# Kernel optimization log

Hardware: AMD Instinct MI355X
Metric: run time of the kernel (lower is better)

Reference implementation:

```python
import jax, jax.numpy as jnp
import numpy as np

B, L, E = 4, 2048, 1024
H, D = 16, 64  # heads, head_dim; H*D == E


def setup_inputs() -> dict:
    key = jax.random.key(0)
    ks = jax.random.split(key, 6)
    s = 0.02
    return {
        "x": jax.random.normal(ks[0], (B, L, E), dtype=jnp.float32),
        "Wq": jax.random.normal(ks[1], (E, H * D), dtype=jnp.float32) * s,
        "Wk": jax.random.normal(ks[2], (E, H * D), dtype=jnp.float32) * s,
        "Wv": jax.random.normal(ks[3], (E, H * D), dtype=jnp.float32) * s,
        "Wo": jax.random.normal(ks[4], (H * D, E), dtype=jnp.float32) * s,
        "bo": jax.random.normal(ks[5], (E,), dtype=jnp.float32) * s,
    }


def reference(x, Wq, Wk, Wv, Wo, bo):
    b, l, e = x.shape
    q = (x @ Wq).reshape(b, l, H, D)
    k = (x @ Wk).reshape(b, l, H, D)
    v = (x @ Wv).reshape(b, l, H, D)
    # NOTE: original scales by sqrt(embed_size), not sqrt(head_dim)
    energy = jnp.einsum('nqhd,nkhd->nhqk', q, k)
    attn = jax.nn.softmax(energy / jnp.sqrt(jnp.float32(e)), axis=3)
    out = jnp.einsum('nhql,nlhd->nqhd', attn, v).reshape(b, l, H * D)
    return out @ Wo + bo
```

## Files before the change

kernel.cpp:

```cpp
#include <hip/hip_runtime.h>

#define B_ 4
#define L_ 2048
#define E_ 1024
#define H_ 16
#define D_ 64
#define CSCALE 0.045084960222629414f

typedef short s16x8 __attribute__((ext_vector_type(8)));
typedef short s16x4 __attribute__((ext_vector_type(4)));
typedef float f32x4 __attribute__((ext_vector_type(4)));

__device__ __forceinline__ unsigned short f2bf(float f) {
  union { float f; unsigned int u; } v;
  v.f = f;
  unsigned int u = v.u;
  u += 0x7fffu + ((u >> 16) & 1u);
  return (unsigned short)(u >> 16);
}

__device__ __forceinline__ void async16(const void* g, void* l) {
  __builtin_amdgcn_global_load_lds(
      (__attribute__((address_space(1))) void*)(g),
      (__attribute__((address_space(3))) void*)(l), 16, 0, 0);
}

__global__ void k_prep(const float* __restrict__ x,
                       const float* __restrict__ Wq, const float* __restrict__ Wk,
                       const float* __restrict__ Wv, const float* __restrict__ Wo,
                       unsigned short* __restrict__ xb,
                       unsigned short* __restrict__ Wt, unsigned short* __restrict__ WoT) {
  __shared__ float t[32][33];
  int bid = blockIdx.x, tid = threadIdx.x;
  if (bid < 8192) {
    int i = bid * 256 + tid;
    float4 v = ((const float4*)x)[i];
    ushort4 o;
    o.x = f2bf(v.x); o.y = f2bf(v.y); o.z = f2bf(v.z); o.w = f2bf(v.w);
    ((ushort4*)xb)[i] = o;
    return;
  }
  int tt = bid - 8192;
  int wsel = tt >> 10, tile = tt & 1023;
  const float* in = (wsel == 0) ? Wq : (wsel == 1) ? Wk : (wsel == 2) ? Wv : Wo;
  unsigned short* out = (wsel == 0) ? Wt : (wsel == 1) ? Wt + (1u << 20)
                        : (wsel == 2) ? Wt + (2u << 20) : WoT;
  int bx = tile & 31, by = tile >> 5;
  int tx = tid & 31, ty = tid >> 5;
  int xcol = bx * 32 + tx;
  int y0 = by * 32;
#pragma unroll
  for (int i = 0; i < 4; ++i)
    t[ty + i * 8][tx] = in[(size_t)(y0 + ty + i * 8) * 1024 + xcol];
  __syncthreads();
  int xo = by * 32 + tx;
  int yo0 = bx * 32;
#pragma unroll
  for (int i = 0; i < 4; ++i)
    out[(size_t)(yo0 + ty + i * 8) * 1024 + xo] = f2bf(t[tx][ty + i * 8]);
}

__global__ __launch_bounds__(512) void k_gemm_qkvt(
    const unsigned short* __restrict__ xb, const unsigned short* __restrict__ Wt,
    unsigned short* __restrict__ Qb, unsigned short* __restrict__ Kb,
    unsigned short* __restrict__ Vt) {
  __shared__ __align__(16) unsigned short St[3][12288];
  const int bid0 = blockIdx.x;
  const int bid = (bid0 & 7) * 96 + (bid0 >> 3);
  const int tid = threadIdx.x;
  const int w = tid >> 6, lane = tid & 63;
  const int quad = lane >> 4, mrow = lane & 15;
  const bool isQK = bid < 512;
  int m0, n0;
  const unsigned short *PA, *PB;
  if (isQK) {
    m0 = (bid & 31) * 256;
    n0 = (bid >> 5) * 128;
    PA = xb + (size_t)m0 * 1024;
    PB = Wt + (size_t)n0 * 1024;
  } else {
    int g = bid - 512;
    m0 = (g & 3) * 256;
    n0 = (g >> 2) * 128;
    PA = Wt + (2u << 20) + (size_t)m0 * 1024;
    PB = xb + (size_t)n0 * 1024;
  }
  const int wr = (w >> 1) * 64, wc = (w & 1) * 64;

  auto issue = [&](int kt, int s) {
    int ktw = kt & 31;
#pragma unroll
    for (int r = 0; r < 2; ++r) {
      int c = r * 512 + tid;
      int row = c >> 2, cl = c & 3, gc = cl ^ (row & 3);
      async16(PA + (size_t)row * 1024 + ktw * 32 + gc * 8, &St[s][c * 8]);
    }
    {
      int c = tid;
      int row = c >> 2, cl = c & 3, gc = cl ^ (row & 3);
      async16(PB + (size_t)row * 1024 + ktw * 32 + gc * 8, &St[s][8192 + c * 8]);
    }
  };

  const f32x4 fz = {0.f, 0.f, 0.f, 0.f};
  f32x4 acc[4][4];
#pragma unroll
  for (int a = 0; a < 4; ++a)
#pragma unroll
    for (int b = 0; b < 4; ++b) acc[a][b] = fz;

  issue(0, 0);
  issue(1, 1);

  for (int kt = 0; kt < 32; ++kt) {
    asm volatile("s_waitcnt vmcnt(3)" ::: "memory");
    __builtin_amdgcn_s_barrier();
    asm volatile("" ::: "memory");
    issue(kt + 2, (kt + 2) % 3);
    const unsigned short* As = &St[kt % 3][0];
    const unsigned short* Bs = &St[kt % 3][8192];
    s16x8 a[4], b[4];
#pragma unroll
    for (int mt = 0; mt < 4; ++mt) {
      int row = wr + mt * 16 + mrow;
      a[mt] = *(const s16x8*)&As[row * 32 + ((quad ^ (row & 3)) << 3)];
    }
#pragma unroll
    for (int nt = 0; nt < 4; ++nt) {
      int row = wc + nt * 16 + mrow;
      b[nt] = *(const s16x8*)&Bs[row * 32 + ((quad ^ (row & 3)) << 3)];
    }
#pragma unroll
    for (int mt = 0; mt < 4; ++mt)
#pragma unroll
      for (int nt = 0; nt < 4; ++nt)
        acc[mt][nt] = __builtin_amdgcn_mfma_f32_16x16x32_bf16(a[mt], b[nt], acc[mt][nt], 0, 0, 0);
  }
  if (isQK) {
#pragma unroll
    for (int mt = 0; mt < 4; ++mt)
#pragma unroll
      for (int nt = 0; nt < 4; ++nt)
#pragma unroll
        for (int i = 0; i < 4; ++i) {
          int row = m0 + wr + mt * 16 + quad * 4 + i;
          int col = n0 + wc + nt * 16 + mrow;
          int bb = row >> 11, l = row & 2047;
          if (col < 1024) {
            int h = col >> 6, d = col & 63;
            Qb[(((size_t)(bb * 16 + h)) * 2048 + l) * 64 + d] = f2bf(acc[mt][nt][i]);
          } else {
            int c2 = col - 1024, h = c2 >> 6, d = c2 & 63;
            Kb[(((size_t)(bb * 16 + h)) * 2048 + l) * 64 + d] = f2bf(acc[mt][nt][i] * CSCALE);
          }
        }
  } else {
#pragma unroll
    for (int mt = 0; mt < 4; ++mt)
#pragma unroll
      for (int nt = 0; nt < 4; ++nt)
#pragma unroll
        for (int i = 0; i < 4; ++i) {
          int f = m0 + wr + mt * 16 + quad * 4 + i;
          int tk = n0 + wc + nt * 16 + mrow;
          int bb = tk >> 11, l = tk & 2047;
          Vt[((size_t)(bb * 1024 + f)) * 2048 + l] = f2bf(acc[mt][nt][i]);
        }
  }
}

struct AK { s16x8 k0, k1; };
struct ST { f32x4 s0, s1; };
struct PAT { s16x4 n0, n1; };

__device__ __forceinline__ AK load_ak(const unsigned short* Kt, int mt, int mrow, int quad) {
  int row = mt * 16 + mrow;
  AK r;
  r.k0 = *(const s16x8*)&Kt[row * 64 + (((0 + quad) ^ (row & 7)) << 3)];
  r.k1 = *(const s16x8*)&Kt[row * 64 + (((4 + quad) ^ (row & 7)) << 3)];
  return r;
}

__device__ __forceinline__ ST qkmm(const AK& a, const s16x8 (&qb)[2][2]) {
  const f32x4 fz = {0.f, 0.f, 0.f, 0.f};
  ST t; t.s0 = fz; t.s1 = fz;
  __builtin_amdgcn_s_setprio(1);
  t.s0 = __builtin_amdgcn_mfma_f32_16x16x32_bf16(a.k0, qb[0][0], t.s0, 0, 0, 0);
  t.s1 = __builtin_amdgcn_mfma_f32_16x16x32_bf16(a.k0, qb[1][0], t.s1, 0, 0, 0);
  t.s0 = __builtin_amdgcn_mfma_f32_16x16x32_bf16(a.k1, qb[0][1], t.s0, 0, 0, 0);
  t.s1 = __builtin_amdgcn_mfma_f32_16x16x32_bf16(a.k1, qb[1][1], t.s1, 0, 0, 0);
  __builtin_amdgcn_s_setprio(0);
  return t;
}

__device__ __forceinline__ s16x4 exp_pack(const f32x4 sv, float& lracc) {
  float p0 = __builtin_amdgcn_exp2f(sv[0]);
  float p1 = __builtin_amdgcn_exp2f(sv[1]);
  float p2 = __builtin_amdgcn_exp2f(sv[2]);
  float p3 = __builtin_amdgcn_exp2f(sv[3]);
  lracc += (p0 + p1) + (p2 + p3);
  unsigned int r01, r23;
  asm("v_cvt_pk_bf16_f32 %0, %1, %2" : "=v"(r01) : "v"(p0), "v"(p1));
  asm("v_cvt_pk_bf16_f32 %0, %1, %2" : "=v"(r23) : "v"(p2), "v"(p3));
  union { unsigned int u[2]; s16x4 v4; } uu;
  uu.u[0] = r01; uu.u[1] = r23;
  return uu.v4;
}

__device__ __forceinline__ PAT expp(const ST& t, float (&lr)[2]) {
  PAT r;
  r.n0 = exp_pack(t.s0, lr[0]);
  r.n1 = exp_pack(t.s1, lr[1]);
  return r;
}

__device__ __forceinline__ void pv(const unsigned short* Vs, int lt, const PAT& p,
                                   f32x4 (&o)[2][4], int mrow, int quad) {
  s16x4 vb[4];
  int lbase = lt * 16 + quad * 4;
  int cg = lbase >> 3, off = lbase & 7;
#pragma unroll
  for (int dt = 0; dt < 4; ++dt) {
    int row = dt * 16 + mrow;
    vb[dt] = *(const s16x4*)&Vs[row * 64 + ((cg ^ (row & 7)) << 3) + off];
  }
  __builtin_amdgcn_s_setprio(1);
#pragma unroll
  for (int dt = 0; dt < 4; ++dt) {
    o[0][dt] = __builtin_amdgcn_mfma_f32_16x16x16bf16_1k(p.n0, vb[dt], o[0][dt], 0, 0, 0);
    o[1][dt] = __builtin_amdgcn_mfma_f32_16x16x16bf16_1k(p.n1, vb[dt], o[1][dt], 0, 0, 0);
  }
  __builtin_amdgcn_s_setprio(0);
}

__global__ __launch_bounds__(512) void k_attn(
    const unsigned short* __restrict__ Qb, const unsigned short* __restrict__ Kb,
    const unsigned short* __restrict__ Vt, unsigned short* __restrict__ AO) {
  __shared__ __align__(16) unsigned short KVs[3][8192];
  const int tid = threadIdx.x, w = tid >> 6, lane = tid & 63;
  const int quad = lane >> 4, mrow = lane & 15;
  const int lin = blockIdx.x + 8 * blockIdx.y;
  const int swz = (lin & 7) * 64 + (lin >> 3);
  const int bh = swz >> 3;
  const int q0 = (swz & 7) * 256;
  const unsigned short* Qh = Qb + (size_t)bh * 2048 * 64;
  const unsigned short* Kh = Kb + (size_t)bh * 2048 * 64;
  const unsigned short* Vh = Vt + (size_t)bh * 64 * 2048;
  unsigned short* KVf = &KVs[0][0];

#pragma unroll
  for (int r = 0; r < 4; ++r) {
    int c = r * 512 + tid;
    int row = c >> 3, cl = c & 7;
    int gc = cl ^ (row & 7);
    async16(Qh + (size_t)(q0 + row) * 64 + gc * 8, &KVf[c * 8]);
  }
  asm volatile("s_waitcnt vmcnt(0)" ::: "memory");
  __builtin_amdgcn_s_barrier();
  asm volatile("" ::: "memory");
  s16x8 qb[2][2];
#pragma unroll
  for (int nt = 0; nt < 2; ++nt)
#pragma unroll
    for (int ks = 0; ks < 2; ++ks) {
      int row = w * 32 + nt * 16 + mrow;
      qb[nt][ks] = *(const s16x8*)&KVf[row * 64 + (((ks * 4 + quad) ^ (row & 7)) << 3)];
    }
  asm volatile("" ::: "memory");
  __builtin_amdgcn_s_barrier();
  asm volatile("" ::: "memory");

  {
    int row = tid >> 3, cl = tid & 7, gc = cl ^ (row & 7);
    async16(Kh + (size_t)row * 64 + gc * 8, &KVs[0][tid * 8]);
    async16(Vh + (size_t)row * 2048 + gc * 8, &KVs[0][4096 + tid * 8]);
    async16(Kh + (size_t)(64 + row) * 64 + gc * 8, &KVs[1][tid * 8]);
    async16(Vh + (size_t)row * 2048 + 64 + gc * 8, &KVs[1][4096 + tid * 8]);
  }

  const f32x4 fz = {0.f, 0.f, 0.f, 0.f};
  f32x4 o[2][4];
  float lr[2];
#pragma unroll
  for (int nt = 0; nt < 2; ++nt) {
    lr[nt] = 0.f;
#pragma unroll
    for (int dt = 0; dt < 4; ++dt) o[nt][dt] = fz;
  }

  for (int j = 0; j < 32; ++j) {
    asm volatile("s_waitcnt vmcnt(2)" ::: "memory");
    __builtin_amdgcn_s_barrier();
    asm volatile("" ::: "memory");
    {
      int jj = (j + 2) & 31;
      unsigned short* nb = &KVs[(j + 2) % 3][0];
      int row = tid >> 3, cl = tid & 7, gc = cl ^ (row & 7);
      async16(Kh + (size_t)(jj * 64 + row) * 64 + gc * 8, &nb[tid * 8]);
      async16(Vh + (size_t)row * 2048 + jj * 64 + gc * 8, &nb[4096 + tid * 8]);
    }
    const unsigned short* Kt = &KVs[j % 3][0];
    const unsigned short* Vs = &KVs[j % 3][4096];

    AK a0 = load_ak(Kt, 0, mrow, quad); ST t0 = qkmm(a0, qb);
    AK a1 = load_ak(Kt, 1, mrow, quad); ST t1 = qkmm(a1, qb);
    PAT p0 = expp(t0, lr);
    AK a2 = load_ak(Kt, 2, mrow, quad); ST t2 = qkmm(a2, qb);
    pv(Vs, 0, p0, o, mrow, quad);
    PAT p1 = expp(t1, lr);
    AK a3 = load_ak(Kt, 3, mrow, quad); ST t3 = qkmm(a3, qb);
    pv(Vs, 1, p1, o, mrow, quad);
    PAT p2 = expp(t2, lr);
    pv(Vs, 2, p2, o, mrow, quad);
    PAT p3 = expp(t3, lr);
    pv(Vs, 3, p3, o, mrow, quad);
  }

#pragma unroll
  for (int nt = 0; nt < 2; ++nt) {
    float v = lr[nt];
    v += __shfl_xor(v, 16);
    v += __shfl_xor(v, 32);
    lr[nt] = v;
  }

  int b_ = bh >> 4, h = bh & 15;
#pragma unroll
  for (int nt = 0; nt < 2; ++nt)
#pragma unroll
    for (int i = 0; i < 4; ++i) {
      float inv = 1.f / __shfl(lr[nt], quad * 4 + i, 64);
      int qrow = q0 + w * 32 + nt * 16 + quad * 4 + i;
#pragma unroll
      for (int dt = 0; dt < 4; ++dt) {
        int d = dt * 16 + mrow;
        AO[((size_t)(b_ * 2048 + qrow)) * 1024 + h * 64 + d] = f2bf(o[nt][dt][i] * inv);
      }
    }
}

__global__ __launch_bounds__(512) void k_gemm_out(
    const unsigned short* __restrict__ Ab, const unsigned short* __restrict__ WoT,
    const float* __restrict__ bo, float* __restrict__ out) {
  __shared__ __align__(16) unsigned short St[3][8192];
  const int tid = threadIdx.x;
  const int w = tid >> 6, lane = tid & 63;
  const int quad = lane >> 4, mrow = lane & 15;
  const int lin = blockIdx.x + 64 * blockIdx.y;
  const int swz = (lin & 7) * 64 + (lin >> 3);
  const int m0 = (swz & 63) * 128, n0 = (swz >> 6) * 128;
  const int wr = (w >> 1) * 32, wc = (w & 1) * 64;
  const unsigned short* PA = Ab + (size_t)m0 * 1024;
  const unsigned short* PB = WoT + (size_t)n0 * 1024;

  auto issue = [&](int kt, int s) {
    int ktw = kt & 31;
    {
      int c = tid;
      int row = c >> 2, cl = c & 3, gc = cl ^ (row & 3);
      async16(PA + (size_t)row * 1024 + ktw * 32 + gc * 8, &St[s][c * 8]);
    }
    {
      int c = tid;
      int row = c >> 2, cl = c & 3, gc = cl ^ (row & 3);
      async16(PB + (size_t)row * 1024 + ktw * 32 + gc * 8, &St[s][4096 + c * 8]);
    }
  };

  const f32x4 fz = {0.f, 0.f, 0.f, 0.f};
  f32x4 acc[2][4];
#pragma unroll
  for (int a = 0; a < 2; ++a)
#pragma unroll
    for (int b = 0; b < 4; ++b) acc[a][b] = fz;

  issue(0, 0);
  issue(1, 1);

  for (int kt = 0; kt < 32; ++kt) {
    asm volatile("s_waitcnt vmcnt(2)" ::: "memory");
    __builtin_amdgcn_s_barrier();
    asm volatile("" ::: "memory");
    issue(kt + 2, (kt + 2) % 3);
    const unsigned short* As = &St[kt % 3][0];
    const unsigned short* Bs = &St[kt % 3][4096];
    s16x8 a[2], b[4];
#pragma unroll
    for (int mt = 0; mt < 2; ++mt) {
      int row = wr + mt * 16 + mrow;
      a[mt] = *(const s16x8*)&As[row * 32 + ((quad ^ (row & 3)) << 3)];
    }
#pragma unroll
    for (int nt = 0; nt < 4; ++nt) {
      int row = wc + nt * 16 + mrow;
      b[nt] = *(const s16x8*)&Bs[row * 32 + ((quad ^ (row & 3)) << 3)];
    }
#pragma unroll
    for (int mt = 0; mt < 2; ++mt)
#pragma unroll
      for (int nt = 0; nt < 4; ++nt)
        acc[mt][nt] = __builtin_amdgcn_mfma_f32_16x16x32_bf16(a[mt], b[nt], acc[mt][nt], 0, 0, 0);
  }
#pragma unroll
  for (int mt = 0; mt < 2; ++mt)
#pragma unroll
    for (int nt = 0; nt < 4; ++nt)
#pragma unroll
      for (int i = 0; i < 4; ++i) {
        int row = m0 + wr + mt * 16 + quad * 4 + i;
        int col = n0 + wc + nt * 16 + mrow;
        out[(size_t)row * 1024 + col] = acc[mt][nt][i] + bo[col];
      }
}

extern "C" void kernel_launch(void* const* d_in, const int* in_sizes, int n_in,
                              void* d_out, int out_size, void* d_ws, size_t ws_size,
                              hipStream_t stream) {
  const float* x  = (const float*)d_in[0];
  const float* Wq = (const float*)d_in[1];
  const float* Wk = (const float*)d_in[2];
  const float* Wv = (const float*)d_in[3];
  const float* Wo = (const float*)d_in[4];
  const float* bo = (const float*)d_in[5];
  float* out = (float*)d_out;

  char* ws = (char*)d_ws;
  const size_t MiB = 1u << 20;
  unsigned short* xb  = (unsigned short*)(ws);
  unsigned short* Wt  = (unsigned short*)(ws + 16 * MiB);
  unsigned short* WoT = (unsigned short*)(ws + 22 * MiB);
  unsigned short* Qb  = (unsigned short*)(ws + 24 * MiB);
  unsigned short* Kb  = (unsigned short*)(ws + 40 * MiB);
  unsigned short* Vt  = (unsigned short*)(ws + 56 * MiB);
  unsigned short* AO  = xb;

  k_prep<<<12288, 256, 0, stream>>>(x, Wq, Wk, Wv, Wo, xb, Wt, WoT);
  k_gemm_qkvt<<<768, 512, 0, stream>>>(xb, Wt, Qb, Kb, Vt);
  k_attn<<<dim3(8, 64), 512, 0, stream>>>(Qb, Kb, Vt, AO);
  k_gemm_out<<<dim3(64, 8), 512, 0, stream>>>(AO, WoT, bo, out);
}
```

Before: 269.0 us.

## Enlarge GEMM tiles to 256x256 and switch LDS to k-chunk-major layout

Both projection GEMMs move to 256x256 output tiles per block, with each wave owning a 128x64 sub-tile (8x4 MFMA accumulators). This raises arithmetic intensity and cuts global reloads of A/B. The LDS staging layout changes from an XOR-swizzled row-major layout to a k-chunk-major layout, and grids shrink accordingly (384 and 128 blocks). The trade-off is heavier register pressure and fewer blocks, which may underfill the 256 CUs, especially for the output GEMM, which now has only 128 blocks.

```diff
diff --git a/kernel.cpp b/kernel.cpp
--- a/kernel.cpp
+++ b/kernel.cpp
@@ -60,52 +60,54 @@
     out[(size_t)(yo0 + ty + i * 8) * 1024 + xo] = f2bf(t[tx][ty + i * 8]);
 }
 
-__global__ __launch_bounds__(512) void k_gemm_qkvt(
+__global__ __launch_bounds__(512, 2) void k_gemm_qkvt(
     const unsigned short* __restrict__ xb, const unsigned short* __restrict__ Wt,
     unsigned short* __restrict__ Qb, unsigned short* __restrict__ Kb,
     unsigned short* __restrict__ Vt) {
-  __shared__ __align__(16) unsigned short St[3][12288];
+  __shared__ __align__(16) unsigned short St[3][16384];
   const int bid0 = blockIdx.x;
-  const int bid = (bid0 & 7) * 96 + (bid0 >> 3);
+  const int bid = (bid0 & 7) * 48 + (bid0 >> 3);
   const int tid = threadIdx.x;
   const int w = tid >> 6, lane = tid & 63;
   const int quad = lane >> 4, mrow = lane & 15;
-  const bool isQK = bid < 512;
+  const bool isQK = bid < 256;
   int m0, n0;
   const unsigned short *PA, *PB;
   if (isQK) {
-    m0 = (bid & 31) * 256;
-    n0 = (bid >> 5) * 128;
+    m0 = (bid >> 3) * 256;
+    n0 = (bid & 7) * 256;
     PA = xb + (size_t)m0 * 1024;
     PB = Wt + (size_t)n0 * 1024;
   } else {
-    int g = bid - 512;
-    m0 = (g & 3) * 256;
-    n0 = (g >> 2) * 128;
+    int g = bid - 256;
+    m0 = (g >> 5) * 256;
+    n0 = (g & 31) * 256;
     PA = Wt + (2u << 20) + (size_t)m0 * 1024;
     PB = xb + (size_t)n0 * 1024;
   }
-  const int wr = (w >> 1) * 64, wc = (w & 1) * 64;
+  const int wr = (w >> 2) * 128;
+  const int wc = (w & 3) * 64;
 
   auto issue = [&](int kt, int s) {
     int ktw = kt & 31;
 #pragma unroll
     for (int r = 0; r < 2; ++r) {
       int c = r * 512 + tid;
-      int row = c >> 2, cl = c & 3, gc = cl ^ (row & 3);
-      async16(PA + (size_t)row * 1024 + ktw * 32 + gc * 8, &St[s][c * 8]);
-    }
-    {
-      int c = tid;
-      int row = c >> 2, cl = c & 3, gc = cl ^ (row & 3);
-      async16(PB + (size_t)row * 1024 + ktw * 32 + gc * 8, &St[s][8192 + c * 8]);
+      int cc = c >> 8, row = c & 255;
+      async16(PA + (size_t)row * 1024 + ktw * 32 + cc * 8, &St[s][c * 8]);
+    }
+#pragma unroll
+    for (int r = 0; r < 2; ++r) {
+      int c = r * 512 + tid;
+      int cc = c >> 8, row = c & 255;
+      async16(PB + (size_t)row * 1024 + ktw * 32 + cc * 8, &St[s][8192 + c * 8]);
     }
   };
 
   const f32x4 fz = {0.f, 0.f, 0.f, 0.f};
-  f32x4 acc[4][4];
-#pragma unroll
-  for (int a = 0; a < 4; ++a)
+  f32x4 acc[8][4];
+#pragma unroll
+  for (int a = 0; a < 8; ++a)
 #pragma unroll
     for (int b = 0; b < 4; ++b) acc[a][b] = fz;
 
@@ -113,32 +115,32 @@
   issue(1, 1);
 
   for (int kt = 0; kt < 32; ++kt) {
-    asm volatile("s_waitcnt vmcnt(3)" ::: "memory");
+    asm volatile("s_waitcnt vmcnt(4)" ::: "memory");
     __builtin_amdgcn_s_barrier();
     asm volatile("" ::: "memory");
     issue(kt + 2, (kt + 2) % 3);
     const unsigned short* As = &St[kt % 3][0];
     const unsigned short* Bs = &St[kt % 3][8192];
-    s16x8 a[4], b[4];
-#pragma unroll
-    for (int mt = 0; mt < 4; ++mt) {
+    s16x8 a[8], b[4];
+#pragma unroll
+    for (int mt = 0; mt < 8; ++mt) {
       int row = wr + mt * 16 + mrow;
-      a[mt] = *(const s16x8*)&As[row * 32 + ((quad ^ (row & 3)) << 3)];
+      a[mt] = *(const s16x8*)&As[(quad * 256 + row) * 8];
     }
 #pragma unroll
     for (int nt = 0; nt < 4; ++nt) {
       int row = wc + nt * 16 + mrow;
-      b[nt] = *(const s16x8*)&Bs[row * 32 + ((quad ^ (row & 3)) << 3)];
-    }
-#pragma unroll
-    for (int mt = 0; mt < 4; ++mt)
+      b[nt] = *(const s16x8*)&Bs[(quad * 256 + row) * 8];
+    }
+#pragma unroll
+    for (int mt = 0; mt < 8; ++mt)
 #pragma unroll
       for (int nt = 0; nt < 4; ++nt)
         acc[mt][nt] = __builtin_amdgcn_mfma_f32_16x16x32_bf16(a[mt], b[nt], acc[mt][nt], 0, 0, 0);
   }
   if (isQK) {
 #pragma unroll
-    for (int mt = 0; mt < 4; ++mt)
+    for (int mt = 0; mt < 8; ++mt)
 #pragma unroll
       for (int nt = 0; nt < 4; ++nt)
 #pragma unroll
@@ -156,7 +158,7 @@
         }
   } else {
 #pragma unroll
-    for (int mt = 0; mt < 4; ++mt)
+    for (int mt = 0; mt < 8; ++mt)
 #pragma unroll
       for (int nt = 0; nt < 4; ++nt)
 #pragma unroll
@@ -339,38 +341,40 @@
     }
 }
 
-__global__ __launch_bounds__(512) void k_gemm_out(
+__global__ __launch_bounds__(512, 2) void k_gemm_out(
     const unsigned short* __restrict__ Ab, const unsigned short* __restrict__ WoT,
     const float* __restrict__ bo, float* __restrict__ out) {
-  __shared__ __align__(16) unsigned short St[3][8192];
+  __shared__ __align__(16) unsigned short St[3][16384];
+  const int bid0 = blockIdx.x;
+  const int bid = (bid0 & 7) * 16 + (bid0 >> 3);
   const int tid = threadIdx.x;
   const int w = tid >> 6, lane = tid & 63;
   const int quad = lane >> 4, mrow = lane & 15;
-  const int lin = blockIdx.x + 64 * blockIdx.y;
-  const int swz = (lin & 7) * 64 + (lin >> 3);
-  const int m0 = (swz & 63) * 128, n0 = (swz >> 6) * 128;
-  const int wr = (w >> 1) * 32, wc = (w & 1) * 64;
+  const int m0 = (bid >> 2) * 256, n0 = (bid & 3) * 256;
+  const int wr = (w >> 2) * 128, wc = (w & 3) * 64;
   const unsigned short* PA = Ab + (size_t)m0 * 1024;
   const unsigned short* PB = WoT + (size_t)n0 * 1024;
 
   auto issue = [&](int kt, int s) {
     int ktw = kt & 31;
-    {
-      int c = tid;
-      int row = c >> 2, cl = c & 3, gc = cl ^ (row & 3);
-      async16(PA + (size_t)row * 1024 + ktw * 32 + gc * 8, &St[s][c * 8]);
-    }
-    {
-      int c = tid;
-      int row = c >> 2, cl = c & 3, gc = cl ^ (row & 3);
-      async16(PB + (size_t)row * 1024 + ktw * 32 + gc * 8, &St[s][4096 + c * 8]);
+#pragma unroll
+    for (int r = 0; r < 2; ++r) {
+      int c = r * 512 + tid;
+      int cc = c >> 8, row = c & 255;
+      async16(PA + (size_t)row * 1024 + ktw * 32 + cc * 8, &St[s][c * 8]);
+    }
+#pragma unroll
+    for (int r = 0; r < 2; ++r) {
+      int c = r * 512 + tid;
+      int cc = c >> 8, row = c & 255;
+      async16(PB + (size_t)row * 1024 + ktw * 32 + cc * 8, &St[s][8192 + c * 8]);
     }
   };
 
   const f32x4 fz = {0.f, 0.f, 0.f, 0.f};
-  f32x4 acc[2][4];
-#pragma unroll
-  for (int a = 0; a < 2; ++a)
+  f32x4 acc[8][4];
+#pragma unroll
+  for (int a = 0; a < 8; ++a)
 #pragma unroll
     for (int b = 0; b < 4; ++b) acc[a][b] = fz;
 
@@ -378,31 +382,31 @@
   issue(1, 1);
 
   for (int kt = 0; kt < 32; ++kt) {
-    asm volatile("s_waitcnt vmcnt(2)" ::: "memory");
+    asm volatile("s_waitcnt vmcnt(4)" ::: "memory");
     __builtin_amdgcn_s_barrier();
     asm volatile("" ::: "memory");
     issue(kt + 2, (kt + 2) % 3);
     const unsigned short* As = &St[kt % 3][0];
-    const unsigned short* Bs = &St[kt % 3][4096];
-    s16x8 a[2], b[4];
-#pragma unroll
-    for (int mt = 0; mt < 2; ++mt) {
+    const unsigned short* Bs = &St[kt % 3][8192];
+    s16x8 a[8], b[4];
+#pragma unroll
+    for (int mt = 0; mt < 8; ++mt) {
       int row = wr + mt * 16 + mrow;
-      a[mt] = *(const s16x8*)&As[row * 32 + ((quad ^ (row & 3)) << 3)];
+      a[mt] = *(const s16x8*)&As[(quad * 256 + row) * 8];
     }
 #pragma unroll
     for (int nt = 0; nt < 4; ++nt) {
       int row = wc + nt * 16 + mrow;
-      b[nt] = *(const s16x8*)&Bs[row * 32 + ((quad ^ (row & 3)) << 3)];
-    }
-#pragma unroll
-    for (int mt = 0; mt < 2; ++mt)
+      b[nt] = *(const s16x8*)&Bs[(quad * 256 + row) * 8];
+    }
+#pragma unroll
+    for (int mt = 0; mt < 8; ++mt)
 #pragma unroll
       for (int nt = 0; nt < 4; ++nt)
         acc[mt][nt] = __builtin_amdgcn_mfma_f32_16x16x32_bf16(a[mt], b[nt], acc[mt][nt], 0, 0, 0);
   }
 #pragma unroll
-  for (int mt = 0; mt < 2; ++mt)
+  for (int mt = 0; mt < 8; ++mt)
 #pragma unroll
     for (int nt = 0; nt < 4; ++nt)
 #pragma unroll
@@ -435,7 +439,7 @@
   unsigned short* AO  = xb;
 
   k_prep<<<12288, 256, 0, stream>>>(x, Wq, Wk, Wv, Wo, xb, Wt, WoT);
-  k_gemm_qkvt<<<768, 512, 0, stream>>>(xb, Wt, Qb, Kb, Vt);
+  k_gemm_qkvt<<<384, 512, 0, stream>>>(xb, Wt, Qb, Kb, Vt);
   k_attn<<<dim3(8, 64), 512, 0, stream>>>(Qb, Kb, Vt, AO);
-  k_gemm_out<<<dim3(64, 8), 512, 0, stream>>>(AO, WoT, bo, out);
-}
+  k_gemm_out<<<128, 512, 0, stream>>>(AO, WoT, bo, out);
+}
```

Result: slower. 313.0 us (+16.4%).
